# Optimization experiments

Hardware: AMD Instinct MI355X
Metric: run time of the kernel (lower is better)

The kernel has to match this reference:

```python
import jax, jax.numpy as jnp
import numpy as np

N, D, H = 4096, 1024, 16
DK = D // H

def setup_inputs() -> dict:
    key = jax.random.key(0)
    k1, k2 = jax.random.split(key)
    X = jax.random.normal(k1, (N, D), dtype=jnp.float32)
    # torch nn.Linear(D, 2D, bias=False): weight [2D, D]; y = x @ W.T. Store as [D, 2D].
    Wqkv = jax.random.normal(k2, (D, 2 * D), dtype=jnp.float32) * (1.0 / np.sqrt(D))
    return {"X": X, "Wqkv": Wqkv}

def reference(X, Wqkv):
    n = X.shape[0]
    proj = X @ Wqkv                      # [N, 2D]
    qk, v = jnp.split(proj, 2, axis=-1)  # each [N, D]
    qk = qk.reshape(n, H, DK)
    v = v.reshape(n, H, DK)
    scale = DK ** 0.5
    scores = jnp.einsum('nhd,mhd->hnm', qk, qk) / scale  # [H, N, N], Q == K
    att = jax.nn.softmax(scores, axis=-1)
    out = jnp.einsum('hnm,mhd->nhd', att, v)              # [N, H, DK]
    return out.reshape(n, D)
```

## Files before the change

kernel.cpp:

```cpp
#include <hip/hip_runtime.h>

typedef unsigned short u16;
typedef unsigned int u32;
typedef __bf16 bf16x8 __attribute__((ext_vector_type(8)));
typedef float f32x4 __attribute__((ext_vector_type(4)));
typedef float f32x16 __attribute__((ext_vector_type(16)));
typedef int i32x2 __attribute__((ext_vector_type(2)));
typedef unsigned int u32x4 __attribute__((ext_vector_type(4)));

#define N_TOK 4096
#define DMODEL 1024
#define NH 16
#define DKH 64

__device__ inline u16 f2bf(float f){
  unsigned u = __float_as_uint(f);
  u += 0x7fffu + ((u >> 16) & 1u);
  return (u16)(u >> 16);
}

__device__ inline float fexp2(float x){ return __builtin_amdgcn_exp2f(x); }

__global__ __launch_bounds__(256) void k_conv(const float* __restrict__ X, u16* __restrict__ Xb,
                                              const float* __restrict__ W, u16* __restrict__ Wt){
  if (blockIdx.x < 4096){
    int i = blockIdx.x*256 + threadIdx.x;
    const float4 v = reinterpret_cast<const float4*>(X)[i];
    ushort4 o; o.x=f2bf(v.x); o.y=f2bf(v.y); o.z=f2bf(v.z); o.w=f2bf(v.w);
    reinterpret_cast<ushort4*>(Xb)[i] = o;
    return;
  }
  __shared__ float tile[64][65];
  const int b2 = blockIdx.x - 4096;
  const int bn = (b2 & 31)*64;
  const int bk = (b2 >> 5)*64;
  const int t = threadIdx.x;
  const int c4 = (t & 15)*4;
  const int r  = t >> 4;
  #pragma unroll
  for (int i=0;i<4;i++){
    int k = r + i*16;
    const float4 v = *reinterpret_cast<const float4*>(&W[(size_t)(bk+k)*2048 + bn + c4]);
    tile[k][c4+0]=v.x; tile[k][c4+1]=v.y; tile[k][c4+2]=v.z; tile[k][c4+3]=v.w;
  }
  __syncthreads();
  #pragma unroll
  for (int i=0;i<4;i++){
    int n = r + i*16;
    ushort4 o;
    o.x = f2bf(tile[c4+0][n]);
    o.y = f2bf(tile[c4+1][n]);
    o.z = f2bf(tile[c4+2][n]);
    o.w = f2bf(tile[c4+3][n]);
    *reinterpret_cast<ushort4*>(&Wt[(size_t)(bn+n)*1024 + bk + c4]) = o;
  }
}

struct GemmShm {
  union {
    struct { u16 As[128*64]; u16 Bs[128*64]; };
    u16 LB[128*136];
  };
};

__global__ __launch_bounds__(256) void k_gemm(const u16* __restrict__ A, const u16* __restrict__ B,
                                              u16* __restrict__ kf_g, u16* __restrict__ vf_g){
  __shared__ alignas(16) GemmShm shm;
  const int bm = blockIdx.y*128, bn = blockIdx.x*128;
  const int tid = threadIdx.x, wid = tid>>6, lane = tid&63;
  const int wr = wid>>1, wc = wid&1;
  const int lr = lane&15, lg = lane>>4;
  f32x4 acc[4][4] = {};

  for (int kk=0; kk<DMODEL; kk+=64){
    __syncthreads();
    #pragma unroll
    for (int i=0;i<4;i++){
      const int chunk = (wid*4+i)*64 + lane;
      const int row = chunk>>3, koc = chunk&7;
      const int swz = koc ^ (row&7);
      const u16* ga = A + (size_t)(bm+row)*DMODEL + kk + swz*8;
      const u16* gb = B + (size_t)(bn+row)*DMODEL + kk + swz*8;
      __builtin_amdgcn_global_load_lds((const __attribute__((address_space(1))) void*)ga,
          (__attribute__((address_space(3))) void*)(&shm.As[(size_t)chunk*8]), 16, 0, 0);
      __builtin_amdgcn_global_load_lds((const __attribute__((address_space(1))) void*)gb,
          (__attribute__((address_space(3))) void*)(&shm.Bs[(size_t)chunk*8]), 16, 0, 0);
    }
    asm volatile("s_waitcnt vmcnt(0)" ::: "memory");
    __syncthreads();
    #pragma unroll
    for (int ks=0; ks<2; ks++){
      bf16x8 af[4], bfr[4];
      #pragma unroll
      for (int m=0;m<4;m++){
        const int row = wr*64+m*16+lr, cr = ks*4+lg;
        af[m] = *reinterpret_cast<const bf16x8*>(&shm.As[(size_t)(row*8 + (cr ^ (row&7)))*8]);
      }
      #pragma unroll
      for (int n=0;n<4;n++){
        const int row = wc*64+n*16+lr, cr = ks*4+lg;
        bfr[n] = *reinterpret_cast<const bf16x8*>(&shm.Bs[(size_t)(row*8 + (cr ^ (row&7)))*8]);
      }
      #pragma unroll
      for (int m=0;m<4;m++)
        #pragma unroll
        for (int n=0;n<4;n++)
          acc[m][n] = __builtin_amdgcn_mfma_f32_16x16x32_bf16(af[m], bfr[n], acc[m][n], 0,0,0);
    }
  }

  if (bn < DMODEL){
    __syncthreads();
    #pragma unroll
    for (int m=0;m<4;m++){
      const int row0 = wr*64 + m*16 + lg*4;
      #pragma unroll
      for (int n=0;n<4;n++){
        const int col = wc*64 + n*16 + lr;
        #pragma unroll
        for (int r=0;r<4;r++)
          shm.LB[(size_t)(row0+r)*136 + col] = f2bf(acc[m][n][r]);
      }
    }
    __syncthreads();
    #pragma unroll
    for (int i=0;i<8;i++){
      const int chunk = i*256 + tid;
      const int hh2  = chunk >> 10;
      const int rem  = chunk & 1023;
      const int kb_l = rem >> 8;
      const int ds   = (rem >> 6) & 3;
      const int l    = rem & 63;
      const int row_local = kb_l*32 + (l & 31);
      const int colbase   = hh2*64 + ds*16 + ((l >> 5) << 3);
      u32x4 v = *reinterpret_cast<const u32x4*>(&shm.LB[(size_t)row_local*136 + colbase]);
      const int hh = (bn>>6) + hh2;
      const int kb = (bm>>5) + kb_l;
      u16* dst = kf_g + (size_t)hh*262144 + ((size_t)kb*4 + ds)*512 + (size_t)l*8;
      *reinterpret_cast<u32x4*>(dst) = v;
    }
  } else {
    #pragma unroll
    for (int m=0;m<4;m++){
      const int row0 = bm + wr*64 + m*16 + lg*4;
      #pragma unroll
      for (int n=0;n<4;n++){
        const int c = bn + wc*64 + n*16 + lr;
        const int cc = c - DMODEL; const int hh = cc>>6, d = cc&63;
        const size_t base = (((size_t)hh*64 + (row0>>6))*8 + (d>>5)*4 + ((row0>>4)&3))*512
                          + (size_t)(((d&31) | (((row0>>3)&1)<<5)))*8 + (row0&7);
        ushort4 o;
        o.x = f2bf(acc[m][n][0]); o.y = f2bf(acc[m][n][1]);
        o.z = f2bf(acc[m][n][2]); o.w = f2bf(acc[m][n][3]);
        *reinterpret_cast<ushort4*>(&vf_g[base]) = o;
      }
    }
  }
}

__device__ inline bf16x8 scale_bf8(bf16x8 v, float s){
  u32x4 w = __builtin_bit_cast(u32x4, v);
  u32x4 r;
  #pragma unroll
  for (int i=0;i<4;i++){
    float lo = __uint_as_float(w[i] << 16) * s;
    float hi = __uint_as_float(w[i] & 0xffff0000u) * s;
    u32 p;
    asm("v_cvt_pk_bf16_f32 %0, %1, %2" : "=v"(p) : "v"(lo), "v"(hi));
    r[i] = p;
  }
  return __builtin_bit_cast(bf16x8, r);
}

__global__ __launch_bounds__(256,2) void k_attn(const u16* __restrict__ kf_g, const u16* __restrict__ vf_g,
                                                float* __restrict__ out){
  __shared__ alignas(16) u16 stg[2][16384];
  const int bid  = blockIdx.x;
  const int xcd  = bid & 7;
  const int slot = bid >> 3;
  const int h    = (xcd<<1) | (slot>>5);
  const int qt   = slot & 31;
  const int wid  = threadIdx.x >> 6;
  const int lane = threadIdx.x & 63;
  const int ql   = lane & 31;
  const int q0   = qt*128 + wid*32;
  const u16* __restrict__ Kfh = kf_g + (size_t)h*262144;
  const u16* __restrict__ Vfh = vf_g + (size_t)h*262144;
  const float SC = 0.18033688011112042f;

  bf16x8 qb[4];
  #pragma unroll
  for (int ds=0; ds<4; ds++){
    bf16x8 raw = *reinterpret_cast<const bf16x8*>(&Kfh[(size_t)((q0>>5)*4 + ds)*512 + lane*8]);
    qb[ds] = scale_bf8(raw, SC);
  }

  f32x16 o0 = {}, o1 = {}, lacc = {};

  auto stage = [&](int buf, int t){
    #pragma unroll
    for (int i=0; i<8; i++){
      const int c = wid + i*4;
      const u16* src = (c < 16)
        ? Kfh + ((size_t)(t*16 + c))*512 + lane*8
        : Vfh + ((size_t)(t*16 + c - 16))*512 + lane*8;
      __builtin_amdgcn_global_load_lds((const __attribute__((address_space(1))) void*)src,
          (__attribute__((address_space(3))) void*)(&stg[buf][(size_t)c*512]), 16, 0, 0);
    }
  };

  stage(0, 0);
  int cur = 0;
  for (int t=0; t<32; ++t){
    asm volatile("s_waitcnt vmcnt(0)" ::: "memory");
    __syncthreads();
    if (t < 31) stage(cur^1, t+1);

    const u16* kb = &stg[cur][0];

    auto QK = [&](int ss, f32x16& p){
      bf16x8 k0 = *reinterpret_cast<const bf16x8*>(&kb[(size_t)(ss*4+0)*512 + lane*8]);
      bf16x8 k1 = *reinterpret_cast<const bf16x8*>(&kb[(size_t)(ss*4+1)*512 + lane*8]);
      bf16x8 k2 = *reinterpret_cast<const bf16x8*>(&kb[(size_t)(ss*4+2)*512 + lane*8]);
      bf16x8 k3 = *reinterpret_cast<const bf16x8*>(&kb[(size_t)(ss*4+3)*512 + lane*8]);
      f32x16 acc = {};
      acc = __builtin_amdgcn_mfma_f32_32x32x16_bf16(k0, qb[0], acc, 0,0,0);
      acc = __builtin_amdgcn_mfma_f32_32x32x16_bf16(k1, qb[1], acc, 0,0,0);
      acc = __builtin_amdgcn_mfma_f32_32x32x16_bf16(k2, qb[2], acc, 0,0,0);
      acc = __builtin_amdgcn_mfma_f32_32x32x16_bf16(k3, qb[3], acc, 0,0,0);
      p = acc;
    };
    auto SM = [&](f32x16& p, u32* pk){
      #pragma unroll
      for (int c=0; c<16; c++) p[c] = fexp2(p[c]);
      lacc += p;
      #pragma unroll
      for (int c2=0; c2<8; c2++){
        u32 a;
        asm("v_cvt_pk_bf16_f32 %0, %1, %2" : "=v"(a) : "v"(p[2*c2]), "v"(p[2*c2+1]));
        pk[c2] = a;
      }
    };
    auto PV = [&](int ss, const u32* pk){
      const int vbase = 8192 + ((ss>>1)*8 + (ss&1)*2)*512;
      bf16x8 va0 = *reinterpret_cast<const bf16x8*>(&kb[(size_t)vbase          + lane*8]);
      bf16x8 va1 = *reinterpret_cast<const bf16x8*>(&kb[(size_t)vbase +   512  + lane*8]);
      bf16x8 vb0 = *reinterpret_cast<const bf16x8*>(&kb[(size_t)vbase + 4*512  + lane*8]);
      bf16x8 vb1 = *reinterpret_cast<const bf16x8*>(&kb[(size_t)vbase + 5*512  + lane*8]);
      #pragma unroll
      for (int t2=0; t2<2; t2++){
        const int base = 4*t2;
        i32x2 r0s = __builtin_amdgcn_permlane32_swap((int)pk[base+0], (int)pk[base+2], false, false);
        i32x2 r1s = __builtin_amdgcn_permlane32_swap((int)pk[base+1], (int)pk[base+3], false, false);
        u32x4 w; w[0] = (u32)r0s[0]; w[1] = (u32)r1s[0]; w[2] = (u32)r0s[1]; w[3] = (u32)r1s[1];
        bf16x8 bt = __builtin_bit_cast(bf16x8, w);
        o0 = __builtin_amdgcn_mfma_f32_32x32x16_bf16(t2 ? va1 : va0, bt, o0, 0,0,0);
        o1 = __builtin_amdgcn_mfma_f32_32x32x16_bf16(t2 ? vb1 : vb0, bt, o1, 0,0,0);
      }
    };

    f32x16 pA, pB;
    u32 pkA[8], pkB[8];
    QK(0, pA);
    QK(1, pB);
    SM(pA, pkA);
    PV(0, pkA);
    QK(2, pA);
    SM(pB, pkB);
    PV(1, pkB);
    QK(3, pB);
    SM(pA, pkA);
    PV(2, pkA);
    SM(pB, pkB);
    PV(3, pkB);

    __syncthreads();
    cur ^= 1;
  }

  float lp = (((lacc[0]+lacc[1])+(lacc[2]+lacc[3])) + ((lacc[4]+lacc[5])+(lacc[6]+lacc[7])))
           + (((lacc[8]+lacc[9])+(lacc[10]+lacc[11])) + ((lacc[12]+lacc[13])+(lacc[14]+lacc[15])));
  lp += __shfl_xor(lp, 32, 64);

  const int hi = lane >> 5;
  const float inv = 1.f / lp;
  float* orow = out + (size_t)(q0 + ql)*DMODEL + h*DKH;
  #pragma unroll
  for (int g=0; g<4; g++){
    float4 s0, s1;
    s0.x = o0[4*g+0]*inv; s0.y = o0[4*g+1]*inv; s0.z = o0[4*g+2]*inv; s0.w = o0[4*g+3]*inv;
    s1.x = o1[4*g+0]*inv; s1.y = o1[4*g+1]*inv; s1.z = o1[4*g+2]*inv; s1.w = o1[4*g+3]*inv;
    *reinterpret_cast<float4*>(&orow[      8*g + 4*hi]) = s0;
    *reinterpret_cast<float4*>(&orow[32 +  8*g + 4*hi]) = s1;
  }
}

extern "C" void kernel_launch(void* const* d_in, const int* in_sizes, int n_in,
                              void* d_out, int out_size, void* d_ws, size_t ws_size,
                              hipStream_t stream) {
  const float* X = (const float*)d_in[0];
  const float* W = (const float*)d_in[1];
  float* out = (float*)d_out;
  u16* Xb = (u16*)d_ws;
  u16* Wt = Xb + (size_t)N_TOK*DMODEL;
  u16* Kf = Wt + (size_t)2*DMODEL*DMODEL;
  u16* Vf = Kf + (size_t)N_TOK*DMODEL;

  k_conv <<<dim3(4608), dim3(256), 0, stream>>>(X, Xb, W, Wt);
  k_gemm <<<dim3(16,32), dim3(256), 0, stream>>>(Xb, Wt, Kf, Vf);
  k_attn <<<dim3(512), dim3(256), 0, stream>>>(Kf, Vf, out);
}
```

Measured before the change: 114.7 us.

## Double-buffer GEMM LDS staging and stage V epilogue through shared memory

The QKV projection GEMM now uses two LDS staging buffers, so the global-to-LDS loads for the next K tile are issued before the MFMA work on the current tile, hiding load latency behind compute. The V-output epilogue now transposes through the LDS scratch buffer and writes 16-byte coalesced chunks in the fragment layout, replacing scattered 8-byte stores. Double buffering doubles the staging LDS footprint, which may reduce occupancy, and adds a barrier per iteration.

```diff
diff --git a/kernel.cpp b/kernel.cpp
--- a/kernel.cpp
+++ b/kernel.cpp
@@ -58,7 +58,7 @@
 
 struct GemmShm {
   union {
-    struct { u16 As[128*64]; u16 Bs[128*64]; };
+    u16 stg[2][16384];
     u16 LB[128*136];
   };
 };
@@ -72,8 +72,7 @@
   const int lr = lane&15, lg = lane>>4;
   f32x4 acc[4][4] = {};
 
-  for (int kk=0; kk<DMODEL; kk+=64){
-    __syncthreads();
+  auto stage = [&](int buf, int kk){
     #pragma unroll
     for (int i=0;i<4;i++){
       const int chunk = (wid*4+i)*64 + lane;
@@ -82,24 +81,32 @@
       const u16* ga = A + (size_t)(bm+row)*DMODEL + kk + swz*8;
       const u16* gb = B + (size_t)(bn+row)*DMODEL + kk + swz*8;
       __builtin_amdgcn_global_load_lds((const __attribute__((address_space(1))) void*)ga,
-          (__attribute__((address_space(3))) void*)(&shm.As[(size_t)chunk*8]), 16, 0, 0);
+          (__attribute__((address_space(3))) void*)(&shm.stg[buf][(size_t)chunk*8]), 16, 0, 0);
       __builtin_amdgcn_global_load_lds((const __attribute__((address_space(1))) void*)gb,
-          (__attribute__((address_space(3))) void*)(&shm.Bs[(size_t)chunk*8]), 16, 0, 0);
-    }
+          (__attribute__((address_space(3))) void*)(&shm.stg[buf][8192 + (size_t)chunk*8]), 16, 0, 0);
+    }
+  };
+
+  stage(0, 0);
+  int cur = 0;
+  for (int t=0; t<16; ++t){
     asm volatile("s_waitcnt vmcnt(0)" ::: "memory");
     __syncthreads();
+    if (t < 15) stage(cur^1, (t+1)*64);
+    const u16* As = &shm.stg[cur][0];
+    const u16* Bs = &shm.stg[cur][8192];
     #pragma unroll
     for (int ks=0; ks<2; ks++){
       bf16x8 af[4], bfr[4];
       #pragma unroll
       for (int m=0;m<4;m++){
         const int row = wr*64+m*16+lr, cr = ks*4+lg;
-        af[m] = *reinterpret_cast<const bf16x8*>(&shm.As[(size_t)(row*8 + (cr ^ (row&7)))*8]);
+        af[m] = *reinterpret_cast<const bf16x8*>(&As[(size_t)(row*8 + (cr ^ (row&7)))*8]);
       }
       #pragma unroll
       for (int n=0;n<4;n++){
         const int row = wc*64+n*16+lr, cr = ks*4+lg;
-        bfr[n] = *reinterpret_cast<const bf16x8*>(&shm.Bs[(size_t)(row*8 + (cr ^ (row&7)))*8]);
+        bfr[n] = *reinterpret_cast<const bf16x8*>(&Bs[(size_t)(row*8 + (cr ^ (row&7)))*8]);
       }
       #pragma unroll
       for (int m=0;m<4;m++)
@@ -107,10 +114,11 @@
         for (int n=0;n<4;n++)
           acc[m][n] = __builtin_amdgcn_mfma_f32_16x16x32_bf16(af[m], bfr[n], acc[m][n], 0,0,0);
     }
+    __syncthreads();
+    cur ^= 1;
   }
 
   if (bn < DMODEL){
-    __syncthreads();
     #pragma unroll
     for (int m=0;m<4;m++){
       const int row0 = wr*64 + m*16 + lg*4;
@@ -142,18 +150,33 @@
   } else {
     #pragma unroll
     for (int m=0;m<4;m++){
-      const int row0 = bm + wr*64 + m*16 + lg*4;
+      const int row0 = wr*64 + m*16 + lg*4;
       #pragma unroll
       for (int n=0;n<4;n++){
-        const int c = bn + wc*64 + n*16 + lr;
-        const int cc = c - DMODEL; const int hh = cc>>6, d = cc&63;
-        const size_t base = (((size_t)hh*64 + (row0>>6))*8 + (d>>5)*4 + ((row0>>4)&3))*512
-                          + (size_t)(((d&31) | (((row0>>3)&1)<<5)))*8 + (row0&7);
+        const int col = wc*64 + n*16 + lr;
         ushort4 o;
         o.x = f2bf(acc[m][n][0]); o.y = f2bf(acc[m][n][1]);
         o.z = f2bf(acc[m][n][2]); o.w = f2bf(acc[m][n][3]);
-        *reinterpret_cast<ushort4*>(&vf_g[base]) = o;
-      }
+        *reinterpret_cast<ushort4*>(&shm.LB[(size_t)col*136 + row0]) = o;
+      }
+    }
+    __syncthreads();
+    const int hh_base = (bn - DMODEL) >> 6;
+    const int kb_base = bm >> 6;
+    #pragma unroll
+    for (int i=0;i<8;i++){
+      const int unit = i*256 + tid;
+      const int l  = unit & 63;
+      const int c5 = unit >> 6;
+      const int hh2  = c5 >> 4;
+      const int kb_l = (c5 >> 3) & 1;
+      const int dt   = (c5 >> 2) & 1;
+      const int tt   = c5 & 3;
+      const int col_local = hh2*64 + dt*32 + (l & 31);
+      const int row_base  = kb_l*64 + tt*16 + ((l >> 5) << 3);
+      u32x4 v = *reinterpret_cast<const u32x4*>(&shm.LB[(size_t)col_local*136 + row_base]);
+      u16* dst = vf_g + ((size_t)((hh_base+hh2)*64 + kb_base + kb_l)*8 + dt*4 + tt)*512 + (size_t)l*8;
+      *reinterpret_cast<u32x4*>(dst) = v;
     }
   }
 }
```

After: 113.6 us. Within noise of the previous version (-0.9%).
